# Performance work log

Hardware: AMD Instinct MI355X
Metric: run time of the kernel (lower is better)

## Reference

```python
import jax, jax.numpy as jnp
import numpy as np

N = 30000      # nodes
E = 480000     # edges (before self-loops)
F_IN = 128     # dim_in
H = 8          # heads
C = 32         # dim_h (per-head channels)
F_H = H * C    # concat hidden width = 256
NEG_SLOPE = 0.2


def setup_inputs() -> dict:
    key = jax.random.key(0)
    ks = jax.random.split(key, 12)
    def glorot(k, shape, fan):
        return jax.random.normal(k, shape, jnp.float32) * (1.0 / np.sqrt(fan))
    return {
        "x": jax.random.normal(ks[0], (N, F_IN), jnp.float32),
        "edge_index": jax.random.randint(ks[1], (2, E), 0, N),
        "W1": glorot(ks[2], (F_IN, F_H), F_IN),
        "a1_src": glorot(ks[3], (H, C), C),
        "a1_dst": glorot(ks[4], (H, C), C),
        "b1": jnp.zeros((F_H,), jnp.float32),
        "W2": glorot(ks[5], (F_H, F_H), F_H),
        "a2_src": glorot(ks[6], (H, C), C),
        "a2_dst": glorot(ks[7], (H, C), C),
        "b2": jnp.zeros((F_H,), jnp.float32),
        "Wl": glorot(ks[8], (F_H, 1), F_H),
        "bl": jnp.zeros((1,), jnp.float32),
    }


def gat_conv(x, src, dst, W, a_src, a_dst, b):
    """PyG-style GATConv (concat=True, add_self_loops handled by caller)."""
    n = x.shape[0]
    h = (x @ W).reshape(n, H, C)                       # [N,H,C]
    alpha_s = jnp.einsum('nhc,hc->nh', h, a_src)        # [N,H]
    alpha_d = jnp.einsum('nhc,hc->nh', h, a_dst)        # [N,H]
    e = jax.nn.leaky_relu(alpha_s[src] + alpha_d[dst], NEG_SLOPE)  # [E,H]
    # segment softmax over incoming edges of each destination node
    e_max = jax.ops.segment_max(e, dst, num_segments=n)            # [N,H]
    e_max = jnp.where(jnp.isfinite(e_max), e_max, 0.0)
    e_exp = jnp.exp(e - e_max[dst])                                # [E,H]
    denom = jax.ops.segment_sum(e_exp, dst, num_segments=n)        # [N,H]
    alpha = e_exp / (denom[dst] + 1e-16)                           # [E,H]
    out = jax.ops.segment_sum(h[src] * alpha[:, :, None], dst, num_segments=n)  # [N,H,C]
    return out.reshape(n, F_H) + b


def reference(x, edge_index, W1, a1_src, a1_dst, b1, W2, a2_src, a2_dst, b2, Wl, bl):
    loops = jnp.arange(N, dtype=edge_index.dtype)      # self-loops (PyG default)
    src = jnp.concatenate([edge_index[0], loops])
    dst = jnp.concatenate([edge_index[1], loops])
    h = jax.nn.elu(gat_conv(x, src, dst, W1, a1_src, a1_dst, b1))
    h = jax.nn.elu(gat_conv(h, src, dst, W2, a2_src, a2_dst, b2))
    return (h @ Wl + bl).squeeze(1)                    # [N]
```

## Files before the change

kernel.cpp:

```cpp
#include <hip/hip_runtime.h>
#include <hip/hip_bf16.h>

#define NNODES 30000
#define NEDGES 480000
#define TE (NEDGES + NNODES)
#define FH 256
#define NH 8
#define NSB ((NNODES + 255) / 256)

typedef unsigned short ushort_t;
typedef __attribute__((ext_vector_type(8))) _Float16 f16x8;
typedef __attribute__((ext_vector_type(2))) _Float16 f16x2;
typedef __attribute__((ext_vector_type(4))) float f32x4;

__global__ void count_kernel(const int* __restrict__ ei, int* __restrict__ counts) {
    int e = blockIdx.x * 256 + threadIdx.x;
    if (e >= TE) return;
    int d = (e < NEDGES) ? ei[NEDGES + e] : (e - NEDGES);
    atomicAdd(&counts[d], 1);
}

__global__ __launch_bounds__(256) void scan1_kernel(const int* __restrict__ counts,
                                                    int* __restrict__ rp,
                                                    int* __restrict__ bsum) {
    __shared__ int s[256];
    const int tid = threadIdx.x;
    const int i = blockIdx.x * 256 + tid;
    int v = (i < NNODES) ? counts[i] : 0;
    s[tid] = v;
    __syncthreads();
    for (int off = 1; off < 256; off <<= 1) {
        int t = (tid >= off) ? s[tid - off] : 0;
        __syncthreads();
        s[tid] += t;
        __syncthreads();
    }
    if (i < NNODES) rp[i] = s[tid] - v;
    if (tid == 255) bsum[blockIdx.x] = s[255];
}

__global__ __launch_bounds__(128) void scan2_kernel(int* __restrict__ bsum) {
    __shared__ int s[128];
    const int tid = threadIdx.x;
    int v = (tid < NSB) ? bsum[tid] : 0;
    s[tid] = v;
    __syncthreads();
    for (int off = 1; off < 128; off <<= 1) {
        int t = (tid >= off) ? s[tid - off] : 0;
        __syncthreads();
        s[tid] += t;
        __syncthreads();
    }
    if (tid < NSB) bsum[tid] = s[tid] - v;
}

__global__ __launch_bounds__(256) void scan3_kernel(int* __restrict__ rp,
                                                    const int* __restrict__ bsum,
                                                    int* __restrict__ cursor) {
    const int i = blockIdx.x * 256 + threadIdx.x;
    if (i < NNODES) {
        int r = rp[i] + bsum[blockIdx.x];
        rp[i] = r;
        cursor[i] = r;
    }
    if (i == 0) rp[NNODES] = TE;
}

__global__ void fill_kernel(const int* __restrict__ ei, int* __restrict__ cursor,
                            int* __restrict__ ssrc) {
    int e = blockIdx.x * 256 + threadIdx.x;
    if (e >= TE) return;
    int s, d;
    if (e < NEDGES) { s = ei[e]; d = ei[NEDGES + e]; }
    else            { s = e - NEDGES; d = s; }
    int pos = atomicAdd(&cursor[d], 1);
    ssrc[pos] = s;
}

__device__ __forceinline__ float2 h2f2(unsigned u) {
    f16x2 h = __builtin_bit_cast(f16x2, u);
    return make_float2((float)h.x, (float)h.y);
}
__device__ __forceinline__ unsigned f2h2(float a, float b) {
    f16x2 h;
    h.x = (_Float16)a;
    h.y = (_Float16)b;
    return __builtin_bit_cast(unsigned, h);
}

__global__ void cvt_x_kernel(const float* __restrict__ X,
                             _Float16* __restrict__ out, int nquads) {
    int i = blockIdx.x * 256 + threadIdx.x;
    if (i >= nquads) return;
    float4 v = *reinterpret_cast<const float4*>(&X[(size_t)i * 4]);
    uint2 st;
    st.x = f2h2(v.x, v.y);
    st.y = f2h2(v.z, v.w);
    *reinterpret_cast<uint2*>(&out[(size_t)i * 4]) = st;
}

template<int K>
__global__ void cvtT_w(const float* __restrict__ W, _Float16* __restrict__ t) {
    int idx = blockIdx.x * 256 + threadIdx.x;
    if (idx >= 256 * K) return;
    int n = idx & 255, k = idx >> 8;
    t[n * K + k] = (_Float16)W[idx];
}

template<int K>
__global__ __launch_bounds__(256) void gemm_mfma(
    const _Float16* __restrict__ A,  const _Float16* __restrict__ Bt,
    const float* __restrict__ ASRC, const float* __restrict__ ADST,
    _Float16* __restrict__ HFh, float* __restrict__ AS, float* __restrict__ AD) {

    constexpr int LDK = 40;
    __shared__ _Float16 Ah[128][LDK], Bh[128][LDK];

    const int tid  = threadIdx.x;
    const int lane = tid & 63;
    const int wid  = tid >> 6;
    const int m0 = blockIdx.x * 128;
    const int n0 = blockIdx.y * 128;
    const int wm = (wid & 1) * 64, wn = (wid >> 1) * 64;
    const int q = lane >> 4;
    const int c = lane & 15;

    f32x4 acc[4][4];
#pragma unroll
    for (int mi = 0; mi < 4; ++mi)
#pragma unroll
        for (int ni = 0; ni < 4; ++ni) acc[mi][ni] = (f32x4){0.f, 0.f, 0.f, 0.f};

    for (int k0 = 0; k0 < K; k0 += 32) {
        __syncthreads();
#pragma unroll
        for (int rep = 0; rep < 2; ++rep) {
            int idx = tid + 256 * rep;
            int row = idx >> 2;
            int ch  = (idx & 3) * 8;
            int gr = m0 + row;
            uint4 v = make_uint4(0u, 0u, 0u, 0u);
            if (gr < NNODES)
                v = *reinterpret_cast<const uint4*>(&A[(size_t)gr * K + k0 + ch]);
            *reinterpret_cast<uint4*>(&Ah[row][ch]) = v;
            uint4 bv = *reinterpret_cast<const uint4*>(&Bt[(size_t)(n0 + row) * K + k0 + ch]);
            *reinterpret_cast<uint4*>(&Bh[row][ch]) = bv;
        }
        __syncthreads();

        const int koff = q * 8;
        f16x8 fa[4], fb[4];
#pragma unroll
        for (int mi = 0; mi < 4; ++mi)
            fa[mi] = *reinterpret_cast<const f16x8*>(&Ah[wm + mi * 16 + c][koff]);
#pragma unroll
        for (int ni = 0; ni < 4; ++ni)
            fb[ni] = *reinterpret_cast<const f16x8*>(&Bh[wn + ni * 16 + c][koff]);
#pragma unroll
        for (int mi = 0; mi < 4; ++mi)
#pragma unroll
            for (int ni = 0; ni < 4; ++ni)
                acc[mi][ni] = __builtin_amdgcn_mfma_f32_16x16x32_f16(fa[mi], fb[ni], acc[mi][ni], 0, 0, 0);
    }

    float as_v[4], ad_v[4];
#pragma unroll
    for (int ni = 0; ni < 4; ++ni) {
        as_v[ni] = ASRC[n0 + wn + ni * 16 + c];
        ad_v[ni] = ADST[n0 + wn + ni * 16 + c];
    }
    const int head0 = (n0 + wn) >> 5;

#pragma unroll
    for (int mi = 0; mi < 4; ++mi) {
#pragma unroll
        for (int j = 0; j < 4; ++j) {
            int row = m0 + wm + mi * 16 + q * 4 + j;
            bool ok = row < NNODES;
            if (ok) {
#pragma unroll
                for (int ni = 0; ni < 4; ++ni)
                    HFh[(size_t)row * FH + n0 + wn + ni * 16 + c] = (_Float16)acc[mi][ni][j];
            }
            float ps0 = acc[mi][0][j] * as_v[0] + acc[mi][1][j] * as_v[1];
            float ps1 = acc[mi][2][j] * as_v[2] + acc[mi][3][j] * as_v[3];
            float pd0 = acc[mi][0][j] * ad_v[0] + acc[mi][1][j] * ad_v[1];
            float pd1 = acc[mi][2][j] * ad_v[2] + acc[mi][3][j] * ad_v[3];
#pragma unroll
            for (int off = 8; off >= 1; off >>= 1) {
                ps0 += __shfl_xor(ps0, off);
                ps1 += __shfl_xor(ps1, off);
                pd0 += __shfl_xor(pd0, off);
                pd1 += __shfl_xor(pd1, off);
            }
            if (ok && c == 0) {
                AS[row * NH + head0]     = ps0;
                AS[row * NH + head0 + 1] = ps1;
                AD[row * NH + head0]     = pd0;
                AD[row * NH + head0 + 1] = pd1;
            }
        }
    }
}

template<bool FINAL>
__global__ __launch_bounds__(256) void aggregate(
    const _Float16* __restrict__ HFh, const float* __restrict__ AS,
    const float* __restrict__ AD,
    const int* __restrict__ rp, const int* __restrict__ ssrc,
    const float* __restrict__ BIAS,
    _Float16* __restrict__ X2H,
    const float* __restrict__ WL, const float* __restrict__ BL,
    float* __restrict__ OUT) {

    const int tid  = threadIdx.x;
    const int lane = tid & 63;
    const int node = __builtin_amdgcn_readfirstlane(blockIdx.x * 4 + (tid >> 6));
    const int epar = lane >> 5;
    const int cg   = lane & 31;
    const int hh   = cg >> 2;
    const int c8   = cg * 8;

    const float ad = AD[node * NH + hh];
    const int p0   = rp[node];
    const int deg  = rp[node + 1] - p0;

    float a0=0.f,a1=0.f,a2=0.f,a3=0.f,a4=0.f,a5=0.f,a6=0.f,a7=0.f;
    float den = 0.f;

#pragma unroll 2
    for (int e0 = 0; e0 < deg; e0 += 2) {
        const int  e   = e0 + epar;
        const bool act = e < deg;
        const int  sa  = ssrc[p0 + (act ? e : 0)];
        const float asv = AS[sa * NH + hh];
        const uint4 hv  = *reinterpret_cast<const uint4*>(&HFh[(size_t)sa * FH + c8]);
        float sv = asv + ad;
        sv = sv > 0.f ? sv : 0.2f * sv;
        const float w = act ? __expf(sv) : 0.f;
        den += w;
        float2 c0 = h2f2(hv.x), c1 = h2f2(hv.y), c2 = h2f2(hv.z), c3 = h2f2(hv.w);
        a0 = fmaf(w, c0.x, a0);
        a1 = fmaf(w, c0.y, a1);
        a2 = fmaf(w, c1.x, a2);
        a3 = fmaf(w, c1.y, a3);
        a4 = fmaf(w, c2.x, a4);
        a5 = fmaf(w, c2.y, a5);
        a6 = fmaf(w, c3.x, a6);
        a7 = fmaf(w, c3.y, a7);
    }

    a0 += __shfl_xor(a0, 32); a1 += __shfl_xor(a1, 32);
    a2 += __shfl_xor(a2, 32); a3 += __shfl_xor(a3, 32);
    a4 += __shfl_xor(a4, 32); a5 += __shfl_xor(a5, 32);
    a6 += __shfl_xor(a6, 32); a7 += __shfl_xor(a7, 32);
    den += __shfl_xor(den, 32);

    const float inv = 1.f / (den + 1e-16f);
    const float4 b0 = *reinterpret_cast<const float4*>(&BIAS[c8]);
    const float4 b1 = *reinterpret_cast<const float4*>(&BIAS[c8 + 4]);
    float o[8];
    o[0] = fmaf(a0, inv, b0.x); o[1] = fmaf(a1, inv, b0.y);
    o[2] = fmaf(a2, inv, b0.z); o[3] = fmaf(a3, inv, b0.w);
    o[4] = fmaf(a4, inv, b1.x); o[5] = fmaf(a5, inv, b1.y);
    o[6] = fmaf(a6, inv, b1.z); o[7] = fmaf(a7, inv, b1.w);
#pragma unroll
    for (int j = 0; j < 8; ++j) o[j] = o[j] > 0.f ? o[j] : expm1f(o[j]);

    if (!FINAL) {
        uint2 st;
        st.x = f2h2(o[epar * 4 + 0], o[epar * 4 + 1]);
        st.y = f2h2(o[epar * 4 + 2], o[epar * 4 + 3]);
        *reinterpret_cast<uint2*>(&X2H[(size_t)node * FH + c8 + epar * 4]) = st;
    } else {
        const float4 w0 = *reinterpret_cast<const float4*>(&WL[c8]);
        const float4 w1 = *reinterpret_cast<const float4*>(&WL[c8 + 4]);
        float pl = fmaf(o[0], w0.x, fmaf(o[1], w0.y, fmaf(o[2], w0.z, o[3] * w0.w)));
        pl = fmaf(o[4], w1.x, fmaf(o[5], w1.y, fmaf(o[6], w1.z, fmaf(o[7], w1.w, pl))));
#pragma unroll
        for (int off = 16; off >= 1; off >>= 1) pl += __shfl_xor(pl, off);
        if (lane == 0) OUT[node] = pl + BL[0];
    }
}

extern "C" void kernel_launch(void* const* d_in, const int* in_sizes, int n_in,
                              void* d_out, int out_size, void* d_ws, size_t ws_size,
                              hipStream_t stream) {
    const float* x   = (const float*)d_in[0];
    const int*   ei  = (const int*)d_in[1];
    const float* W1  = (const float*)d_in[2];
    const float* a1s = (const float*)d_in[3];
    const float* a1d = (const float*)d_in[4];
    const float* b1  = (const float*)d_in[5];
    const float* W2  = (const float*)d_in[6];
    const float* a2s = (const float*)d_in[7];
    const float* a2d = (const float*)d_in[8];
    const float* b2  = (const float*)d_in[9];
    const float* Wl  = (const float*)d_in[10];
    const float* bl  = (const float*)d_in[11];
    float* out = (float*)d_out;

    char* w = (char*)d_ws;
    auto alloc = [&](size_t bytes) -> char* {
        char* p = w;
        w += (bytes + 255) & ~size_t(255);
        return p;
    };
    int*   counts = (int*)alloc((size_t)NNODES * 4);
    int*   rp     = (int*)alloc((size_t)(NNODES + 1) * 4);
    int*   cursor = (int*)alloc((size_t)NNODES * 4);
    int*   bsum   = (int*)alloc((size_t)NSB * 4);
    int*   ssrc   = (int*)alloc((size_t)TE * 4);
    _Float16* hfh = (_Float16*)alloc((size_t)NNODES * FH * 2);
    _Float16* x1h = (_Float16*)alloc((size_t)NNODES * 128 * 2);
    _Float16* x2h = (_Float16*)alloc((size_t)NNODES * FH * 2);
    float* asb    = (float*)alloc((size_t)NNODES * NH * 4);
    float* adb    = (float*)alloc((size_t)NNODES * NH * 4);
    _Float16* w1t = (_Float16*)alloc((size_t)128 * 256 * 2);
    _Float16* w2t = (_Float16*)alloc((size_t)256 * 256 * 2);

    hipMemsetAsync(counts, 0, (size_t)NNODES * 4, stream);
    count_kernel<<<(TE + 255) / 256, 256, 0, stream>>>(ei, counts);
    scan1_kernel<<<NSB, 256, 0, stream>>>(counts, rp, bsum);
    scan2_kernel<<<1, 128, 0, stream>>>(bsum);
    scan3_kernel<<<NSB, 256, 0, stream>>>(rp, bsum, cursor);
    fill_kernel<<<(TE + 255) / 256, 256, 0, stream>>>(ei, cursor, ssrc);

    const int xq = NNODES * 128 / 4;
    cvt_x_kernel<<<(xq + 255) / 256, 256, 0, stream>>>(x, x1h, xq);
    cvtT_w<128><<<128, 256, 0, stream>>>(W1, w1t);
    cvtT_w<256><<<256, 256, 0, stream>>>(W2, w2t);

    const dim3 ggrid((NNODES + 127) / 128, 2);
    gemm_mfma<128><<<ggrid, 256, 0, stream>>>(x1h, w1t, a1s, a1d, hfh, asb, adb);
    aggregate<false><<<NNODES / 4, 256, 0, stream>>>(hfh, asb, adb, rp, ssrc, b1,
                                                     x2h, nullptr, nullptr, nullptr);
    gemm_mfma<256><<<ggrid, 256, 0, stream>>>(x2h, w2t, a2s, a2d, hfh, asb, adb);
    aggregate<true><<<NNODES / 4, 256, 0, stream>>>(hfh, asb, adb, rp, ssrc, b2,
                                                    nullptr, Wl, bl, out);
}
```

Before: 198.9 us.

## Precompute normalized attention coefficients in separate per-edge kernel before aggregation

Adds an alpha_kernel that computes leaky-relu exp scores per edge and normalizes them per destination node using wave reductions, storing an [E,8] float alpha buffer. The aggregate kernel then reads the precomputed weight instead of gathering AS and computing exp, and drops the running denominator. The aggregate loop unroll rises from 2 to 4. The split trades in-loop exp and gather work for an extra kernel launch per layer and additional global memory traffic for the alpha buffer.

After: 217.1 us. +9.1%, slower.

```diff
diff --git a/kernel.cpp b/kernel.cpp
--- a/kernel.cpp
+++ b/kernel.cpp
@@ -77,10 +77,6 @@
     ssrc[pos] = s;
 }
 
-__device__ __forceinline__ float2 h2f2(unsigned u) {
-    f16x2 h = __builtin_bit_cast(f16x2, u);
-    return make_float2((float)h.x, (float)h.y);
-}
 __device__ __forceinline__ unsigned f2h2(float a, float b) {
     f16x2 h;
     h.x = (_Float16)a;
@@ -203,10 +199,95 @@
     }
 }
 
+__global__ __launch_bounds__(256) void alpha_kernel(
+    const float* __restrict__ AS, const float* __restrict__ AD,
+    const int* __restrict__ rp, const int* __restrict__ ssrc,
+    float* __restrict__ ALPHA) {
+
+    const int tid  = threadIdx.x;
+    const int lane = tid & 63;
+    const int node = __builtin_amdgcn_readfirstlane(blockIdx.x * 4 + (tid >> 6));
+
+    const int p0  = rp[node];
+    const int deg = rp[node + 1] - p0;
+
+    const float4 ad0 = *reinterpret_cast<const float4*>(&AD[node * NH]);
+    const float4 ad1 = *reinterpret_cast<const float4*>(&AD[node * NH + 4]);
+
+    if (deg <= 64) {
+        float w[8];
+#pragma unroll
+        for (int h = 0; h < 8; ++h) w[h] = 0.f;
+        if (lane < deg) {
+            int s = ssrc[p0 + lane];
+            float4 as0 = *reinterpret_cast<const float4*>(&AS[s * NH]);
+            float4 as1 = *reinterpret_cast<const float4*>(&AS[s * NH + 4]);
+            float sv[8] = {as0.x + ad0.x, as0.y + ad0.y, as0.z + ad0.z, as0.w + ad0.w,
+                           as1.x + ad1.x, as1.y + ad1.y, as1.z + ad1.z, as1.w + ad1.w};
+#pragma unroll
+            for (int h = 0; h < 8; ++h) {
+                float t = sv[h] > 0.f ? sv[h] : 0.2f * sv[h];
+                w[h] = __expf(t);
+            }
+        }
+        float den[8];
+#pragma unroll
+        for (int h = 0; h < 8; ++h) {
+            den[h] = w[h];
+#pragma unroll
+            for (int off = 32; off >= 1; off >>= 1)
+                den[h] += __shfl_xor(den[h], off);
+        }
+        if (lane < deg) {
+            float4 o0, o1;
+            o0.x = w[0] / (den[0] + 1e-16f); o0.y = w[1] / (den[1] + 1e-16f);
+            o0.z = w[2] / (den[2] + 1e-16f); o0.w = w[3] / (den[3] + 1e-16f);
+            o1.x = w[4] / (den[4] + 1e-16f); o1.y = w[5] / (den[5] + 1e-16f);
+            o1.z = w[6] / (den[6] + 1e-16f); o1.w = w[7] / (den[7] + 1e-16f);
+            *reinterpret_cast<float4*>(&ALPHA[(size_t)(p0 + lane) * NH])     = o0;
+            *reinterpret_cast<float4*>(&ALPHA[(size_t)(p0 + lane) * NH + 4]) = o1;
+        }
+    } else {
+        float den[8];
+#pragma unroll
+        for (int h = 0; h < 8; ++h) den[h] = 0.f;
+        for (int e = lane; e < deg; e += 64) {
+            int s = ssrc[p0 + e];
+            float4 as0 = *reinterpret_cast<const float4*>(&AS[s * NH]);
+            float4 as1 = *reinterpret_cast<const float4*>(&AS[s * NH + 4]);
+            float sv[8] = {as0.x + ad0.x, as0.y + ad0.y, as0.z + ad0.z, as0.w + ad0.w,
+                           as1.x + ad1.x, as1.y + ad1.y, as1.z + ad1.z, as1.w + ad1.w};
+            float w[8];
+#pragma unroll
+            for (int h = 0; h < 8; ++h) {
+                float t = sv[h] > 0.f ? sv[h] : 0.2f * sv[h];
+                w[h] = __expf(t);
+                den[h] += w[h];
+            }
+            *reinterpret_cast<float4*>(&ALPHA[(size_t)(p0 + e) * NH])     = make_float4(w[0], w[1], w[2], w[3]);
+            *reinterpret_cast<float4*>(&ALPHA[(size_t)(p0 + e) * NH + 4]) = make_float4(w[4], w[5], w[6], w[7]);
+        }
+#pragma unroll
+        for (int h = 0; h < 8; ++h) {
+#pragma unroll
+            for (int off = 32; off >= 1; off >>= 1)
+                den[h] += __shfl_xor(den[h], off);
+            den[h] = 1.f / (den[h] + 1e-16f);
+        }
+        for (int e = lane; e < deg; e += 64) {
+            float4 w0 = *reinterpret_cast<const float4*>(&ALPHA[(size_t)(p0 + e) * NH]);
+            float4 w1 = *reinterpret_cast<const float4*>(&ALPHA[(size_t)(p0 + e) * NH + 4]);
+            w0.x *= den[0]; w0.y *= den[1]; w0.z *= den[2]; w0.w *= den[3];
+            w1.x *= den[4]; w1.y *= den[5]; w1.z *= den[6]; w1.w *= den[7];
+            *reinterpret_cast<float4*>(&ALPHA[(size_t)(p0 + e) * NH])     = w0;
+            *reinterpret_cast<float4*>(&ALPHA[(size_t)(p0 + e) * NH + 4]) = w1;
+        }
+    }
+}
+
 template<bool FINAL>
 __global__ __launch_bounds__(256) void aggregate(
-    const _Float16* __restrict__ HFh, const float* __restrict__ AS,
-    const float* __restrict__ AD,
+    const _Float16* __restrict__ HFh, const float* __restrict__ ALPHA,
     const int* __restrict__ rp, const int* __restrict__ ssrc,
     const float* __restrict__ BIAS,
     _Float16* __restrict__ X2H,
@@ -221,49 +302,40 @@
     const int hh   = cg >> 2;
     const int c8   = cg * 8;
 
-    const float ad = AD[node * NH + hh];
-    const int p0   = rp[node];
-    const int deg  = rp[node + 1] - p0;
+    const int p0  = rp[node];
+    const int deg = rp[node + 1] - p0;
 
     float a0=0.f,a1=0.f,a2=0.f,a3=0.f,a4=0.f,a5=0.f,a6=0.f,a7=0.f;
-    float den = 0.f;
-
-#pragma unroll 2
+
+#pragma unroll 4
     for (int e0 = 0; e0 < deg; e0 += 2) {
         const int  e   = e0 + epar;
         const bool act = e < deg;
-        const int  sa  = ssrc[p0 + (act ? e : 0)];
-        const float asv = AS[sa * NH + hh];
-        const uint4 hv  = *reinterpret_cast<const uint4*>(&HFh[(size_t)sa * FH + c8]);
-        float sv = asv + ad;
-        sv = sv > 0.f ? sv : 0.2f * sv;
-        const float w = act ? __expf(sv) : 0.f;
-        den += w;
-        float2 c0 = h2f2(hv.x), c1 = h2f2(hv.y), c2 = h2f2(hv.z), c3 = h2f2(hv.w);
-        a0 = fmaf(w, c0.x, a0);
-        a1 = fmaf(w, c0.y, a1);
-        a2 = fmaf(w, c1.x, a2);
-        a3 = fmaf(w, c1.y, a3);
-        a4 = fmaf(w, c2.x, a4);
-        a5 = fmaf(w, c2.y, a5);
-        a6 = fmaf(w, c3.x, a6);
-        a7 = fmaf(w, c3.y, a7);
+        const int  idx = p0 + (act ? e : 0);
+        const int  sa  = ssrc[idx];
+        const float wr = ALPHA[(size_t)idx * NH + hh];
+        const float w  = act ? wr : 0.f;
+        const f16x8 hv = *reinterpret_cast<const f16x8*>(&HFh[(size_t)sa * FH + c8]);
+        a0 = fmaf((float)hv[0], w, a0);
+        a1 = fmaf((float)hv[1], w, a1);
+        a2 = fmaf((float)hv[2], w, a2);
+        a3 = fmaf((float)hv[3], w, a3);
+        a4 = fmaf((float)hv[4], w, a4);
+        a5 = fmaf((float)hv[5], w, a5);
+        a6 = fmaf((float)hv[6], w, a6);
+        a7 = fmaf((float)hv[7], w, a7);
     }
 
     a0 += __shfl_xor(a0, 32); a1 += __shfl_xor(a1, 32);
     a2 += __shfl_xor(a2, 32); a3 += __shfl_xor(a3, 32);
     a4 += __shfl_xor(a4, 32); a5 += __shfl_xor(a5, 32);
     a6 += __shfl_xor(a6, 32); a7 += __shfl_xor(a7, 32);
-    den += __shfl_xor(den, 32);
-
-    const float inv = 1.f / (den + 1e-16f);
+
     const float4 b0 = *reinterpret_cast<const float4*>(&BIAS[c8]);
     const float4 b1 = *reinterpret_cast<const float4*>(&BIAS[c8 + 4]);
     float o[8];
-    o[0] = fmaf(a0, inv, b0.x); o[1] = fmaf(a1, inv, b0.y);
-    o[2] = fmaf(a2, inv, b0.z); o[3] = fmaf(a3, inv, b0.w);
-    o[4] = fmaf(a4, inv, b1.x); o[5] = fmaf(a5, inv, b1.y);
-    o[6] = fmaf(a6, inv, b1.z); o[7] = fmaf(a7, inv, b1.w);
+    o[0] = a0 + b0.x; o[1] = a1 + b0.y; o[2] = a2 + b0.z; o[3] = a3 + b0.w;
+    o[4] = a4 + b1.x; o[5] = a5 + b1.y; o[6] = a6 + b1.z; o[7] = a7 + b1.w;
 #pragma unroll
     for (int j = 0; j < 8; ++j) o[j] = o[j] > 0.f ? o[j] : expm1f(o[j]);
 
@@ -311,6 +383,7 @@
     int*   cursor = (int*)alloc((size_t)NNODES * 4);
     int*   bsum   = (int*)alloc((size_t)NSB * 4);
     int*   ssrc   = (int*)alloc((size_t)TE * 4);
+    float* alpha  = (float*)alloc((size_t)TE * NH * 4);
     _Float16* hfh = (_Float16*)alloc((size_t)NNODES * FH * 2);
     _Float16* x1h = (_Float16*)alloc((size_t)NNODES * 128 * 2);
     _Float16* x2h = (_Float16*)alloc((size_t)NNODES * FH * 2);
@@ -333,9 +406,11 @@
 
     const dim3 ggrid((NNODES + 127) / 128, 2);
     gemm_mfma<128><<<ggrid, 256, 0, stream>>>(x1h, w1t, a1s, a1d, hfh, asb, adb);
-    aggregate<false><<<NNODES / 4, 256, 0, stream>>>(hfh, asb, adb, rp, ssrc, b1,
+    alpha_kernel<<<NNODES / 4, 256, 0, stream>>>(asb, adb, rp, ssrc, alpha);
+    aggregate<false><<<NNODES / 4, 256, 0, stream>>>(hfh, alpha, rp, ssrc, b1,
                                                      x2h, nullptr, nullptr, nullptr);
     gemm_mfma<256><<<ggrid, 256, 0, stream>>>(x2h, w2t, a2s, a2d, hfh, asb, adb);
-    aggregate<true><<<NNODES / 4, 256, 0, stream>>>(hfh, asb, adb, rp, ssrc, b2,
+    alpha_kernel<<<NNODES / 4, 256, 0, stream>>>(asb, adb, rp, ssrc, alpha);
+    aggregate<true><<<NNODES / 4, 256, 0, stream>>>(hfh, alpha, rp, ssrc, b2,
                                                     nullptr, Wl, bl, out);
 }
```
